# Kernel tuning notes

Measured on AMD Instinct MI355X. Metric: run time of the kernel, lower is better.

## Reference

```python
import jax, jax.numpy as jnp
import numpy as np

# static multi-scale pyramid (must match spatial_shapes array in setup_inputs)
SPATIAL = ((100, 100), (50, 50), (25, 25), (13, 13))
E, H, L, P = 256, 8, 4, 8   # embed_dims, num_heads, num_levels, num_points
BS, NQ = 2, 10000
LEN_VAL = sum(h * w for h, w in SPATIAL)


def _bilinear_gather(val, grid, Hs, Ws):
    """val: [BH, Hs*Ws, d]; grid: [BH, N, 2] in [-1,1].
    Matches F.grid_sample(mode='bilinear', padding_mode='zeros', align_corners=False)."""
    x = (grid[..., 0] + 1.0) * (Ws * 0.5) - 0.5
    y = (grid[..., 1] + 1.0) * (Hs * 0.5) - 0.5
    x0 = jnp.floor(x).astype(jnp.int32)
    y0 = jnp.floor(y).astype(jnp.int32)
    x1, y1 = x0 + 1, y0 + 1
    wx1 = x - x0.astype(x.dtype)
    wy1 = y - y0.astype(y.dtype)
    wx0, wy0 = 1.0 - wx1, 1.0 - wy1

    def corner(xi, yi, w):
        valid = (xi >= 0) & (xi < Ws) & (yi >= 0) & (yi < Hs)
        idx = jnp.clip(yi, 0, Hs - 1) * Ws + jnp.clip(xi, 0, Ws - 1)  # [BH, N]
        v = jnp.take_along_axis(val, idx[..., None], axis=1)          # [BH, N, d]
        return v * (w * valid.astype(w.dtype))[..., None]

    return (corner(x0, y0, wx0 * wy0) + corner(x1, y0, wx1 * wy0)
            + corner(x0, y1, wx0 * wy1) + corner(x1, y1, wx1 * wy1))


def setup_inputs() -> dict:
    key = jax.random.key(0)
    ks = jax.random.split(key, 10)
    scale = 1.0 / np.sqrt(E)
    inp = {
        'query': jax.random.normal(ks[0], (BS, NQ, E), jnp.float32),
        'value': jax.random.normal(ks[1], (BS, LEN_VAL, E), jnp.float32),
        'query_pos': 0.1 * jax.random.normal(ks[2], (BS, NQ, E), jnp.float32),
        'reference_points': jax.random.uniform(ks[3], (BS, NQ, L, 2), jnp.float32),
        'spatial_shapes': jnp.array(SPATIAL, dtype=jnp.int32),
        'W_off': 0.02 * jax.random.normal(ks[4], (E, H * L * P * 2), jnp.float32),
        'b_off': 0.5 * jax.random.normal(ks[5], (H * L * P * 2,), jnp.float32),
        'W_attn': 0.02 * jax.random.normal(ks[6], (E, H * L * P), jnp.float32),
        'b_attn': jnp.zeros((H * L * P,), jnp.float32),
        'W_val': scale * jax.random.normal(ks[7], (E, E), jnp.float32),
        'b_val': jnp.zeros((E,), jnp.float32),
        'W_out': scale * jax.random.normal(ks[8], (E, E), jnp.float32),
        'b_out': jnp.zeros((E,), jnp.float32),
    }
    return inp


def reference(query, value, query_pos, reference_points, spatial_shapes,
              W_off, b_off, W_attn, b_attn, W_val, b_val, W_out, b_out):
    d = E // H
    q = query + query_pos                                        # [bs, nq, E]
    bs, nq, _ = q.shape
    v = (value @ W_val + b_val).reshape(bs, LEN_VAL, H, d)       # [bs, len, H, d]
    off = (q @ W_off + b_off).reshape(bs, nq, H, L, P, 2)
    aw = jax.nn.softmax((q @ W_attn + b_attn).reshape(bs, nq, H, L * P), axis=-1)
    aw = aw.reshape(bs, nq, H, L, P)
    # normalizer is (W, H) per level
    norm = jnp.stack([spatial_shapes[:, 1], spatial_shapes[:, 0]], -1).astype(q.dtype)
    loc = reference_points[:, :, None, :, None, :] + off / norm[None, None, None, :, None, :]
    grids = 2.0 * loc - 1.0                                      # [bs, nq, H, L, P, 2]

    out = jnp.zeros((bs, nq, H, d), q.dtype)
    start = 0
    for lvl, (Hs, Ws) in enumerate(SPATIAL):
        v_l = v[:, start:start + Hs * Ws]                        # [bs, HW, H, d]
        start += Hs * Ws
        v_l = v_l.transpose(0, 2, 1, 3).reshape(bs * H, Hs * Ws, d)
        g_l = grids[:, :, :, lvl].transpose(0, 2, 1, 3, 4).reshape(bs * H, nq * P, 2)
        s = _bilinear_gather(v_l, g_l, Hs, Ws).reshape(bs, H, nq, P, d)
        w_l = aw[:, :, :, lvl].transpose(0, 2, 1, 3)             # [bs, H, nq, P]
        out = out + jnp.einsum('bhnpc,bhnp->bnhc', s, w_l)
    return out.reshape(bs, nq, E) @ W_out + b_out
```

## Files before the change

### kernel.cpp

```cpp
#include <hip/hip_runtime.h>


#define EE   256
#define HH   8
#define LL   4
#define NQq  10000
#define BSB  2
#define LENV 13294
#define MQ   16
#define ROWS_V (BSB * LENV)

typedef unsigned short u16;
typedef unsigned int   u32;
typedef __attribute__((ext_vector_type(8))) short bf16x8;
typedef __attribute__((ext_vector_type(4))) float f32x4;

__device__ __forceinline__ u32 bf16_of(float f) {
  u32 u = __float_as_uint(f);
  return (u + 0x7FFFu + ((u >> 16) & 1u)) >> 16;
}
__device__ __forceinline__ float bf2f(u32 u) { return __uint_as_float(u << 16); }

__device__ __forceinline__ uint4 pack8(const float* f) {
  uint4 u;
  u.x = bf16_of(f[0]) | (bf16_of(f[1]) << 16);
  u.y = bf16_of(f[2]) | (bf16_of(f[3]) << 16);
  u.z = bf16_of(f[4]) | (bf16_of(f[5]) << 16);
  u.w = bf16_of(f[6]) | (bf16_of(f[7]) << 16);
  return u;
}

__global__ __launch_bounds__(64) void k_prep(
    const float* __restrict__ W_off, const float* __restrict__ W_attn,
    const float* __restrict__ W_val, const float* __restrict__ W_out,
    u16* __restrict__ wcat, u16* __restrict__ wval, u16* __restrict__ wout) {
  const int tile = blockIdx.x >> 3, s = blockIdx.x & 7;
  const int l = threadIdx.x, quad = l >> 4, r16 = l & 15;
  float f[8];
  u16* dst;
  if (tile < 48) {
    int col = tile * 16 + r16;
#pragma unroll
    for (int j = 0; j < 8; ++j) {
      int k = s * 32 + quad * 8 + j;
      f[j] = (col < 512) ? W_off[k * 512 + col] : W_attn[k * 256 + (col - 512)];
    }
    dst = wcat + ((tile * 8 + s) * 64 + l) * 8;
  } else if (tile < 64) {
    int col = (tile - 48) * 16 + r16;
#pragma unroll
    for (int j = 0; j < 8; ++j) f[j] = W_val[(s * 32 + quad * 8 + j) * 256 + col];
    dst = wval + (((tile - 48) * 8 + s) * 64 + l) * 8;
  } else {
    int col = (tile - 64) * 16 + r16;
#pragma unroll
    for (int j = 0; j < 8; ++j) f[j] = W_out[(s * 32 + quad * 8 + j) * 256 + col];
    dst = wout + (((tile - 64) * 8 + s) * 64 + l) * 8;
  }
  *(uint4*)dst = pack8(f);
}

__global__ __launch_bounds__(256) void k_valproj(
    const float* __restrict__ value, const float* __restrict__ b_val,
    const u16* __restrict__ wval, u16* __restrict__ v_ws) {
  __shared__ __align__(16) u16 sA[64][264];
  const int tid = threadIdx.x;
  const int g0 = blockIdx.x * 64;
#pragma unroll
  for (int ch = 0; ch < 8; ++ch) {
    int fidx = ch * 2048 + tid * 8;
    int row = fidx >> 8, col = fidx & 255;
    int g = g0 + row;
    float fv[8] = {0.f, 0.f, 0.f, 0.f, 0.f, 0.f, 0.f, 0.f};
    if (g < ROWS_V) {
      float4 a = *(const float4*)(value + (long)g * 256 + col);
      float4 b = *(const float4*)(value + (long)g * 256 + col + 4);
      fv[0] = a.x; fv[1] = a.y; fv[2] = a.z; fv[3] = a.w;
      fv[4] = b.x; fv[5] = b.y; fv[6] = b.z; fv[7] = b.w;
    }
    *(uint4*)&sA[row][col] = pack8(fv);
  }
  __syncthreads();
  const int wave = tid >> 6, lane = tid & 63, quad = lane >> 4, r16 = lane & 15;
  f32x4 acc[4][4] = {};
  for (int s = 0; s < 8; ++s) {
    bf16x8 af[4];
#pragma unroll
    for (int mt = 0; mt < 4; ++mt)
      af[mt] = *(const bf16x8*)&sA[mt * 16 + r16][s * 32 + quad * 8];
#pragma unroll
    for (int nt = 0; nt < 4; ++nt) {
      bf16x8 bfg = *(const bf16x8*)(wval + (((wave * 4 + nt) * 8 + s) * 64 + lane) * 8);
#pragma unroll
      for (int mt = 0; mt < 4; ++mt)
        acc[nt][mt] = __builtin_amdgcn_mfma_f32_16x16x32_bf16(af[mt], bfg, acc[nt][mt], 0, 0, 0);
    }
  }
  __syncthreads();
#pragma unroll
  for (int nt = 0; nt < 4; ++nt) {
    int col = (wave * 4 + nt) * 16 + r16;
    float bias = b_val[col];
#pragma unroll
    for (int mt = 0; mt < 4; ++mt)
#pragma unroll
      for (int rr = 0; rr < 4; ++rr)
        sA[mt * 16 + quad * 4 + rr][col] = (u16)bf16_of(acc[nt][mt][rr] + bias);
  }
  __syncthreads();
  const int h = tid >> 5, c = tid & 31;
  for (int r = 0; r < 64; ++r) {
    int g = g0 + r;
    if (g >= ROWS_V) break;
    int b = g / LENV, pix = g - b * LENV;
    v_ws[((b * 8 + h) * LENV + pix) * 32 + c] = sA[r][tid];
  }
}

__global__ __launch_bounds__(512, 4) void k_attn(
    const float* __restrict__ query, const float* __restrict__ query_pos,
    const float* __restrict__ refpts,
    const float* __restrict__ b_off, const float* __restrict__ b_attn,
    const float* __restrict__ b_out,
    const u16* __restrict__ wcat, const u16* __restrict__ wout,
    const u16* __restrict__ v_ws, float* __restrict__ out) {
  __shared__ __align__(16) char smem[65536];
  u16   (*sQ)[264]  = (u16(*)[264])smem;
  float (*sC)[772]  = (float(*)[772])smem;
  uint4 (*sTab)[256] = (uint4(*)[256])smem;
  u16   (*sO)[264]  = (u16(*)[264])smem;

  const int tid = threadIdx.x;
  const int g0 = blockIdx.x * MQ;
  const int b = g0 / NQq;
  const int q0 = g0 - b * NQq;
  const int wave = tid >> 6, lane = tid & 63, quad = lane >> 4, r16 = lane & 15;

  {
    int fidx = tid * 8;
    int row = fidx >> 8, col = fidx & 255;
    long base = ((long)(b * NQq + q0 + row)) * 256 + col;
    float4 a0 = *(const float4*)(query + base);
    float4 a1 = *(const float4*)(query + base + 4);
    float4 p0 = *(const float4*)(query_pos + base);
    float4 p1 = *(const float4*)(query_pos + base + 4);
    float fv[8] = {a0.x + p0.x, a0.y + p0.y, a0.z + p0.z, a0.w + p0.w,
                   a1.x + p1.x, a1.y + p1.y, a1.z + p1.z, a1.w + p1.w};
    *(uint4*)&sQ[row][col] = pack8(fv);
  }
  __syncthreads();

  f32x4 acc[6] = {};
  for (int s = 0; s < 8; ++s) {
    bf16x8 af = *(const bf16x8*)&sQ[r16][s * 32 + quad * 8];
#pragma unroll
    for (int t6 = 0; t6 < 6; ++t6) {
      int tile = wave * 6 + t6;
      bf16x8 bfg = *(const bf16x8*)(wcat + ((tile * 8 + s) * 64 + lane) * 8);
      acc[t6] = __builtin_amdgcn_mfma_f32_16x16x32_bf16(af, bfg, acc[t6], 0, 0, 0);
    }
  }
  __syncthreads();
#pragma unroll
  for (int t6 = 0; t6 < 6; ++t6) {
    int col = (wave * 6 + t6) * 16 + r16;
#pragma unroll
    for (int rr = 0; rr < 4; ++rr)
      sC[quad * 4 + rr][col] = acc[t6][rr];
  }
  __syncthreads();

  if (tid < MQ * HH) {
    int m = tid >> 3, h = tid & 7;
    float* p = &sC[m][512 + h * 32];
    const float* ba = b_attn + h * 32;
    float mx = -1e30f;
    for (int j = 0; j < 32; ++j) { float v = p[j] + ba[j]; p[j] = v; mx = fmaxf(mx, v); }
    float sum = 0.f;
    for (int j = 0; j < 32; ++j) { float e = __expf(p[j] - mx); p[j] = e; sum += e; }
    float inv = 1.f / sum;
    for (int j = 0; j < 32; ++j) p[j] *= inv;
  }
  __syncthreads();

  uint4 recs[8];
  {
    const int s = tid & 255, mh = tid >> 8;
    const int l = (s >> 3) & 3;
    const int WlI[4] = {100, 50, 25, 13};
    const int baseI[4] = {0, 10000, 12500, 13125};
    const int Wl = WlI[l], Hl = WlI[l], base = baseI[l];
    const float WlF = (float)Wl;
    const float box = b_off[2 * s], boy = b_off[2 * s + 1];
#pragma unroll
    for (int mm = 0; mm < 8; ++mm) {
      int m = mh * 8 + mm;
      float w = sC[m][512 + s];
      float ax = sC[m][2 * s], ay = sC[m][2 * s + 1];
      float2 rp = *(const float2*)(refpts + (((long)(b * NQq + q0 + m)) * LL + l) * 2);
      float x = rp.x * WlF + (ax + box) - 0.5f;
      float y = rp.y * WlF + (ay + boy) - 0.5f;
      float fx0 = floorf(x), fy0 = floorf(y);
      int x0 = (int)fx0, y0 = (int)fy0;
      float fx = x - fx0, fy = y - fy0;
      bool xv0 = (x0 >= 0) & (x0 < Wl);
      bool xv1 = (x0 >= -1) & (x0 < Wl - 1);
      bool yv0 = (y0 >= 0) & (y0 < Hl);
      bool yv1 = (y0 >= -1) & (y0 < Hl - 1);
      float w00 = w * (1.f - fx) * (1.f - fy) * (float)(xv0 & yv0);
      float w01 = w * fx * (1.f - fy) * (float)(xv1 & yv0);
      float w10 = w * (1.f - fx) * fy * (float)(xv0 & yv1);
      float w11 = w * fx * fy * (float)(xv1 & yv1);
      int x0c = min(max(x0, 0), Wl - 1);
      int x1c = min(max(x0 + 1, 0), Wl - 1);
      int y0c = min(max(y0, 0), Hl - 1);
      int y1c = min(max(y0 + 1, 0), Hl - 1);
      u32 o00 = (u32)(base + y0c * Wl + x0c) * 32u;
      u32 dx = (u32)(x1c - x0c) * 32u;
      u32 dy = (u32)(y1c - y0c) * (u32)Wl * 32u;
      uint4 rec;
      rec.x = bf16_of(w00) | (bf16_of(w01) << 16);
      rec.y = bf16_of(w10) | (bf16_of(w11) << 16);
      rec.z = o00;
      rec.w = (dx << 16) | dy;
      recs[mm] = rec;
    }
  }
  __syncthreads();
  {
    const int s = tid & 255, mh = tid >> 8;
#pragma unroll
    for (int mm = 0; mm < 8; ++mm) sTab[mh * 8 + mm][s] = recs[mm];
  }
  __syncthreads();

  const int half = tid >> 8, h = (tid >> 5) & 7, c = tid & 31;
  float oacc[8] = {};
  {
    const u32 hcb = ((u32)(b * 8 + h) * (u32)LENV) * 32u + (u32)c;
    for (int i = 0; i < 32; ++i) {
      int srow = h * 32 + i;
#pragma unroll
      for (int mm = 0; mm < 8; ++mm) {
        uint4 r = sTab[half * 8 + mm][srow];
        float w00 = __uint_as_float(r.x << 16);
        float w01 = __uint_as_float(r.x & 0xFFFF0000u);
        float w10 = __uint_as_float(r.y << 16);
        float w11 = __uint_as_float(r.y & 0xFFFF0000u);
        u32 dx = r.w >> 16, dy = r.w & 0xFFFFu;
        u32 o00 = hcb + r.z;
        float v00 = bf2f((u32)v_ws[o00]);
        float v01 = bf2f((u32)v_ws[o00 + dx]);
        float v10 = bf2f((u32)v_ws[o00 + dy]);
        float v11 = bf2f((u32)v_ws[o00 + dx + dy]);
        oacc[mm] += w00 * v00 + w01 * v01 + w10 * v10 + w11 * v11;
      }
    }
  }
  __syncthreads();
#pragma unroll
  for (int mm = 0; mm < 8; ++mm)
    sO[half * 8 + mm][h * 32 + c] = (u16)bf16_of(oacc[mm]);
  __syncthreads();

  f32x4 acc2[2] = {};
  for (int s = 0; s < 8; ++s) {
    bf16x8 af = *(const bf16x8*)&sO[r16][s * 32 + quad * 8];
#pragma unroll
    for (int t2 = 0; t2 < 2; ++t2) {
      int tile = wave * 2 + t2;
      bf16x8 bfg = *(const bf16x8*)(wout + ((tile * 8 + s) * 64 + lane) * 8);
      acc2[t2] = __builtin_amdgcn_mfma_f32_16x16x32_bf16(af, bfg, acc2[t2], 0, 0, 0);
    }
  }
#pragma unroll
  for (int t2 = 0; t2 < 2; ++t2) {
    int col = (wave * 2 + t2) * 16 + r16;
    float bias = b_out[col];
#pragma unroll
    for (int rr = 0; rr < 4; ++rr) {
      int row = quad * 4 + rr;
      out[((long)(b * NQq + q0 + row)) * 256 + col] = acc2[t2][rr] + bias;
    }
  }
}

extern "C" void kernel_launch(void* const* d_in, const int* in_sizes, int n_in,
                              void* d_out, int out_size, void* d_ws, size_t ws_size,
                              hipStream_t stream) {
  const float* query     = (const float*)d_in[0];
  const float* value     = (const float*)d_in[1];
  const float* query_pos = (const float*)d_in[2];
  const float* refpts    = (const float*)d_in[3];
  const float* W_off     = (const float*)d_in[5];
  const float* b_off     = (const float*)d_in[6];
  const float* W_attn    = (const float*)d_in[7];
  const float* b_attn    = (const float*)d_in[8];
  const float* W_val     = (const float*)d_in[9];
  const float* b_val     = (const float*)d_in[10];
  const float* W_out     = (const float*)d_in[11];
  const float* b_out     = (const float*)d_in[12];
  float* out = (float*)d_out;

  char* ws = (char*)d_ws;
  u16* v_ws = (u16*)ws;
  u16* wcat = (u16*)(ws + 13613056);
  u16* wval = (u16*)(ws + 13613056 + 393216);
  u16* wout = (u16*)(ws + 13613056 + 393216 + 131072);

  k_prep<<<dim3(80 * 8), dim3(64), 0, stream>>>(W_off, W_attn, W_val, W_out,
                                                wcat, wval, wout);
  k_valproj<<<dim3((ROWS_V + 63) / 64), dim3(256), 0, stream>>>(value, b_val, wval, v_ws);
  k_attn<<<dim3(BSB * NQq / MQ), dim3(512), 0, stream>>>(
      query, query_pos, refpts, b_off, b_attn, b_out, wcat, wout, v_ws, out);
}
```

Baseline: 265.7 us.

## Vectorize bilinear gathers to 4 channels per thread and compact sampling table

The sampling loop is reorganized so each thread loads 4 bf16 channels (8 bytes) per corner instead of one 2-byte element. The sampling table is split into a weight array and a packed offset word with dx/dy flag bits and padded stride 257. This cuts shared memory use, and the per-level row stride is recomputed in-loop. Softmax now uses all threads with shuffle reductions, and the value-projection scatter writes 16-byte vectors instead of scalar u16 stores. These changes aim to reduce gather instruction count and scattered narrow memory traffic, at the cost of fewer queries per thread in the gather loop.

```diff
diff --git a/kernel.cpp b/kernel.cpp
--- a/kernel.cpp
+++ b/kernel.cpp
@@ -19,7 +19,8 @@
   u32 u = __float_as_uint(f);
   return (u + 0x7FFFu + ((u >> 16) & 1u)) >> 16;
 }
-__device__ __forceinline__ float bf2f(u32 u) { return __uint_as_float(u << 16); }
+__device__ __forceinline__ float bflo(u32 u) { return __uint_as_float(u << 16); }
+__device__ __forceinline__ float bfhi(u32 u) { return __uint_as_float(u & 0xFFFF0000u); }
 
 __device__ __forceinline__ uint4 pack8(const float* f) {
   uint4 u;
@@ -66,19 +67,19 @@
   __shared__ __align__(16) u16 sA[64][264];
   const int tid = threadIdx.x;
   const int g0 = blockIdx.x * 64;
-#pragma unroll
+#pragma unroll 2
   for (int ch = 0; ch < 8; ++ch) {
-    int fidx = ch * 2048 + tid * 8;
-    int row = fidx >> 8, col = fidx & 255;
+    int row = ch * 8 + (tid >> 5);
+    int col = (tid & 31) * 8;
     int g = g0 + row;
-    float fv[8] = {0.f, 0.f, 0.f, 0.f, 0.f, 0.f, 0.f, 0.f};
+    uint4 pk = {0u, 0u, 0u, 0u};
     if (g < ROWS_V) {
       float4 a = *(const float4*)(value + (long)g * 256 + col);
-      float4 b = *(const float4*)(value + (long)g * 256 + col + 4);
-      fv[0] = a.x; fv[1] = a.y; fv[2] = a.z; fv[3] = a.w;
-      fv[4] = b.x; fv[5] = b.y; fv[6] = b.z; fv[7] = b.w;
-    }
-    *(uint4*)&sA[row][col] = pack8(fv);
+      float4 c = *(const float4*)(value + (long)g * 256 + col + 4);
+      float fv[8] = {a.x, a.y, a.z, a.w, c.x, c.y, c.z, c.w};
+      pk = pack8(fv);
+    }
+    *(uint4*)&sA[row][col] = pk;
   }
   __syncthreads();
   const int wave = tid >> 6, lane = tid & 63, quad = lane >> 4, r16 = lane & 15;
@@ -108,12 +109,21 @@
         sA[mt * 16 + quad * 4 + rr][col] = (u16)bf16_of(acc[nt][mt][rr] + bias);
   }
   __syncthreads();
-  const int h = tid >> 5, c = tid & 31;
-  for (int r = 0; r < 64; ++r) {
-    int g = g0 + r;
-    if (g >= ROWS_V) break;
-    int b = g / LENV, pix = g - b * LENV;
-    v_ws[((b * 8 + h) * LENV + pix) * 32 + c] = sA[r][tid];
+  {
+    int r0 = tid >> 5;
+    int col = (tid & 31) * 8;
+    int h = col >> 5, c = col & 31;
+#pragma unroll 2
+    for (int p = 0; p < 8; ++p) {
+      int r = p * 8 + r0;
+      int g = g0 + r;
+      if (g < ROWS_V) {
+        int bb = (g >= LENV) ? 1 : 0;
+        int pix = g - (bb ? LENV : 0);
+        *(uint4*)(v_ws + (((long)(bb * 8 + h) * LENV + pix) * 32 + c)) =
+            *(const uint4*)&sA[r][col];
+      }
+    }
   }
 }
 
@@ -124,11 +134,12 @@
     const float* __restrict__ b_out,
     const u16* __restrict__ wcat, const u16* __restrict__ wout,
     const u16* __restrict__ v_ws, float* __restrict__ out) {
-  __shared__ __align__(16) char smem[65536];
-  u16   (*sQ)[264]  = (u16(*)[264])smem;
-  float (*sC)[772]  = (float(*)[772])smem;
-  uint4 (*sTab)[256] = (uint4(*)[256])smem;
-  u16   (*sO)[264]  = (u16(*)[264])smem;
+  __shared__ __align__(16) char smem[49536];
+  u16   (*sQ)[264] = (u16(*)[264])smem;
+  float (*sC)[772] = (float(*)[772])smem;
+  uint2* sWt = (uint2*)smem;
+  u32*   sOf = (u32*)(smem + 32888);
+  u16   (*sO)[264] = (u16(*)[264])smem;
 
   const int tid = threadIdx.x;
   const int g0 = blockIdx.x * MQ;
@@ -137,8 +148,7 @@
   const int wave = tid >> 6, lane = tid & 63, quad = lane >> 4, r16 = lane & 15;
 
   {
-    int fidx = tid * 8;
-    int row = fidx >> 8, col = fidx & 255;
+    int row = tid >> 5, col = (tid & 31) * 8;
     long base = ((long)(b * NQq + q0 + row)) * 256 + col;
     float4 a0 = *(const float4*)(query + base);
     float4 a1 = *(const float4*)(query + base + 4);
@@ -170,20 +180,29 @@
   }
   __syncthreads();
 
-  if (tid < MQ * HH) {
-    int m = tid >> 3, h = tid & 7;
-    float* p = &sC[m][512 + h * 32];
-    const float* ba = b_attn + h * 32;
+  {
+    int m = tid >> 5, h = (tid >> 2) & 7, j = tid & 3;
+    float* p = &sC[m][512 + h * 32 + j * 8];
+    const float* ba = b_attn + h * 32 + j * 8;
+    float v[8];
     float mx = -1e30f;
-    for (int j = 0; j < 32; ++j) { float v = p[j] + ba[j]; p[j] = v; mx = fmaxf(mx, v); }
+#pragma unroll
+    for (int k = 0; k < 8; ++k) { v[k] = p[k] + ba[k]; mx = fmaxf(mx, v[k]); }
+    mx = fmaxf(mx, __shfl_xor(mx, 1));
+    mx = fmaxf(mx, __shfl_xor(mx, 2));
     float sum = 0.f;
-    for (int j = 0; j < 32; ++j) { float e = __expf(p[j] - mx); p[j] = e; sum += e; }
+#pragma unroll
+    for (int k = 0; k < 8; ++k) { v[k] = __expf(v[k] - mx); sum += v[k]; }
+    sum += __shfl_xor(sum, 1);
+    sum += __shfl_xor(sum, 2);
     float inv = 1.f / sum;
-    for (int j = 0; j < 32; ++j) p[j] *= inv;
-  }
-  __syncthreads();
-
-  uint4 recs[8];
+#pragma unroll
+    for (int k = 0; k < 8; ++k) p[k] = v[k] * inv;
+  }
+  __syncthreads();
+
+  uint2 wts[8];
+  u32 obs[8];
   {
     const int s = tid & 255, mh = tid >> 8;
     const int l = (s >> 3) & 3;
@@ -216,51 +235,69 @@
       int y0c = min(max(y0, 0), Hl - 1);
       int y1c = min(max(y0 + 1, 0), Hl - 1);
       u32 o00 = (u32)(base + y0c * Wl + x0c) * 32u;
-      u32 dx = (u32)(x1c - x0c) * 32u;
-      u32 dy = (u32)(y1c - y0c) * (u32)Wl * 32u;
-      uint4 rec;
-      rec.x = bf16_of(w00) | (bf16_of(w01) << 16);
-      rec.y = bf16_of(w10) | (bf16_of(w11) << 16);
-      rec.z = o00;
-      rec.w = (dx << 16) | dy;
-      recs[mm] = rec;
+      u32 dxb = (x1c > x0c) ? 1u : 0u;
+      u32 dyb = (y1c > y0c) ? 1u : 0u;
+      wts[mm].x = bf16_of(w00) | (bf16_of(w01) << 16);
+      wts[mm].y = bf16_of(w10) | (bf16_of(w11) << 16);
+      obs[mm] = o00 | (dxb << 31) | (dyb << 30);
     }
   }
   __syncthreads();
   {
     const int s = tid & 255, mh = tid >> 8;
 #pragma unroll
-    for (int mm = 0; mm < 8; ++mm) sTab[mh * 8 + mm][s] = recs[mm];
-  }
-  __syncthreads();
-
-  const int half = tid >> 8, h = (tid >> 5) & 7, c = tid & 31;
-  float oacc[8] = {};
-  {
-    const u32 hcb = ((u32)(b * 8 + h) * (u32)LENV) * 32u + (u32)c;
-    for (int i = 0; i < 32; ++i) {
-      int srow = h * 32 + i;
-#pragma unroll
-      for (int mm = 0; mm < 8; ++mm) {
-        uint4 r = sTab[half * 8 + mm][srow];
-        float w00 = __uint_as_float(r.x << 16);
-        float w01 = __uint_as_float(r.x & 0xFFFF0000u);
-        float w10 = __uint_as_float(r.y << 16);
-        float w11 = __uint_as_float(r.y & 0xFFFF0000u);
-        u32 dx = r.w >> 16, dy = r.w & 0xFFFFu;
-        u32 o00 = hcb + r.z;
-        float v00 = bf2f((u32)v_ws[o00]);
-        float v01 = bf2f((u32)v_ws[o00 + dx]);
-        float v10 = bf2f((u32)v_ws[o00 + dy]);
-        float v11 = bf2f((u32)v_ws[o00 + dx + dy]);
-        oacc[mm] += w00 * v00 + w01 * v01 + w10 * v10 + w11 * v11;
+    for (int mm = 0; mm < 8; ++mm) {
+      int idx = (mh * 8 + mm) * 257 + s;
+      sWt[idx] = wts[mm];
+      sOf[idx] = obs[mm];
+    }
+  }
+  __syncthreads();
+
+  const int h = tid >> 6, mg = (tid >> 3) & 7, cq = tid & 7;
+  float oacc[2][4] = {};
+  {
+    const u32 hcb = ((u32)(b * 8 + h) * (u32)LENV) * 32u + (u32)(cq * 4);
+    const int WlI[4] = {100, 50, 25, 13};
+#pragma unroll
+    for (int lvl = 0; lvl < 4; ++lvl) {
+      const u32 dyv = (u32)WlI[lvl] * 32u;
+      for (int ii = 0; ii < 8; ++ii) {
+        int sbase = h * 32 + lvl * 8 + ii;
+#pragma unroll
+        for (int mm = 0; mm < 2; ++mm) {
+          int idx = (mg * 2 + mm) * 257 + sbase;
+          uint2 wr = sWt[idx];
+          u32 ob = sOf[idx];
+          u32 o00 = hcb + (ob & 0x000FFFFFu);
+          u32 dx = (ob & 0x80000000u) ? 32u : 0u;
+          u32 dy = (ob & 0x40000000u) ? dyv : 0u;
+          uint2 v00 = *(const uint2*)(v_ws + o00);
+          uint2 v01 = *(const uint2*)(v_ws + o00 + dx);
+          uint2 v10 = *(const uint2*)(v_ws + o00 + dy);
+          uint2 v11 = *(const uint2*)(v_ws + o00 + dx + dy);
+          float w00 = bflo(wr.x), w01 = bfhi(wr.x);
+          float w10 = bflo(wr.y), w11 = bfhi(wr.y);
+          oacc[mm][0] += w00 * bflo(v00.x) + w01 * bflo(v01.x) + w10 * bflo(v10.x) + w11 * bflo(v11.x);
+          oacc[mm][1] += w00 * bfhi(v00.x) + w01 * bfhi(v01.x) + w10 * bfhi(v10.x) + w11 * bfhi(v11.x);
+          oacc[mm][2] += w00 * bflo(v00.y) + w01 * bflo(v01.y) + w10 * bflo(v10.y) + w11 * bflo(v11.y);
+          oacc[mm][3] += w00 * bfhi(v00.y) + w01 * bfhi(v01.y) + w10 * bfhi(v10.y) + w11 * bfhi(v11.y);
+        }
       }
     }
   }
   __syncthreads();
-#pragma unroll
-  for (int mm = 0; mm < 8; ++mm)
-    sO[half * 8 + mm][h * 32 + c] = (u16)bf16_of(oacc[mm]);
+  {
+    int col = h * 32 + cq * 4;
+#pragma unroll
+    for (int mm = 0; mm < 2; ++mm) {
+      int m = mg * 2 + mm;
+      u32 p0 = bf16_of(oacc[mm][0]) | (bf16_of(oacc[mm][1]) << 16);
+      u32 p1 = bf16_of(oacc[mm][2]) | (bf16_of(oacc[mm][3]) << 16);
+      *(u32*)&sO[m][col] = p0;
+      *(u32*)&sO[m][col + 2] = p1;
+    }
+  }
   __syncthreads();
 
   f32x4 acc2[2] = {};
```

New measurement: 752.0 us. +183.0%, slower.
